# Kernel optimization log

Hardware: AMD Instinct MI355X
Metric: run time of the kernel (lower is better)

Reference implementation:

```python
import jax, jax.numpy as jnp
import numpy as np

N, E, DN, DE, H = 50000, 800000, 64, 64, 128


def setup_inputs() -> dict:
    key = jax.random.key(0)
    ks = jax.random.split(key, 12)
    s = 0.05
    return {
        "h": jax.random.normal(ks[0], (N, DN), jnp.float32),
        "eh": jax.random.normal(ks[1], (E, DE), jnp.float32),
        "W_node1": jax.random.normal(ks[2], (DN, H), jnp.float32) * s,
        "b_node1": jax.random.normal(ks[3], (H,), jnp.float32) * s,
        "W_node2": jax.random.normal(ks[4], (H, H), jnp.float32) * s,
        "W_edge1": jax.random.normal(ks[5], (DE, H), jnp.float32) * s,
        "b_edge1": jax.random.normal(ks[6], (H,), jnp.float32) * s,
        "W_edge2": jax.random.normal(ks[7], (H, H), jnp.float32) * s,
        "W_comb": jax.random.normal(ks[8], (H, DN), jnp.float32) * s,
        "W_ue": jax.random.normal(ks[9], (DN, DE), jnp.float32) * s,
        "src": jax.random.randint(ks[10], (E,), 0, N, jnp.int32),
        "dst": jax.random.randint(ks[11], (E,), 0, N, jnp.int32),
    }


def reference(h, eh, W_node1, b_node1, W_node2, W_edge1, b_edge1, W_edge2, W_comb, W_ue, src, dst):
    # gather per-edge endpoint node features: [E, DN]
    hs = h[src]
    hd = h[dst]
    # edge update: h_e = 0.8*h_e + 0.2 * fc_update_edge(h_src * h_dst)
    eh_new = 0.8 * eh + 0.2 * ((hs * hd) @ W_ue)
    # message: two small MLPs then tanh-combine, all per edge
    m1 = jax.nn.relu(hs @ W_node1 + b_node1) @ W_node2       # [E, H]
    m2 = jax.nn.relu(eh_new @ W_edge1 + b_edge1) @ W_edge2   # [E, H]
    m = jnp.tanh((m1 * m2) @ W_comb)                          # [E, DN]
    # reduce: scatter-sum messages to destination nodes + residual
    agg = jax.ops.segment_sum(m, dst, num_segments=h.shape[0])
    return agg + h
```

## Files before the change

kernel.cpp:

```cpp
#include <hip/hip_runtime.h>
#include <hip/hip_bf16.h>

#define NN 50000
#define NE 800000
#define DNODE 64
#define HD 128

typedef __attribute__((ext_vector_type(8)))  short bf16x8;
typedef __attribute__((ext_vector_type(16))) float f32x16;
typedef __attribute__((ext_vector_type(4)))  float f32x4;
typedef __attribute__((ext_vector_type(4)))  unsigned short u16x4;

__device__ __forceinline__ short f2bf(float f) {
    __hip_bfloat16 b = __float2bfloat16(f);
    unsigned short u;
    __builtin_memcpy(&u, &b, 2);
    return (short)u;
}
__device__ __forceinline__ float bf2f(unsigned short s) {
    return __uint_as_float(((unsigned)s) << 16);
}
__device__ __forceinline__ f32x16 zero16() {
    f32x16 z;
#pragma unroll
    for (int i = 0; i < 16; ++i) z[i] = 0.f;
    return z;
}

__device__ __forceinline__ unsigned cvt_pk(float lo, float hi) {
    unsigned r;
    asm("v_cvt_pk_bf16_f32 %0, %1, %2" : "=v"(r) : "v"(lo), "v"(hi));
    return r;
}

__device__ __forceinline__ bf16x8 pack_swap(const float* v) {
    unsigned w0 = cvt_pk(v[0], v[1]);
    unsigned w1 = cvt_pk(v[2], v[3]);
    unsigned w2 = cvt_pk(v[4], v[5]);
    unsigned w3 = cvt_pk(v[6], v[7]);
    asm("v_permlane32_swap_b32 %0, %1" : "+v"(w0), "+v"(w2));
    asm("v_permlane32_swap_b32 %0, %1" : "+v"(w1), "+v"(w3));
    union { unsigned u[4]; bf16x8 f; } o;
    o.u[0] = w0; o.u[1] = w1; o.u[2] = w2; o.u[3] = w3;
    return o.f;
}

__device__ __forceinline__ void build_frags(const float* __restrict__ W, int ncols,
                                            int nks, int nct, bf16x8* dst,
                                            int tid, int nthr) {
    int total = nct * nks * 64;
    for (int p = tid; p < total; p += nthr) {
        int fi = p >> 6, l = p & 63;
        int ct = fi / nks, ks = fi - ct * nks;
        int col = 32 * ct + (l & 31);
        int kb  = 16 * ks + 8 * (l >> 5);
        bf16x8 v;
#pragma unroll
        for (int j = 0; j < 8; ++j) v[j] = f2bf(W[(size_t)(kb + j) * ncols + col]);
        dst[p] = v;
    }
}

__global__ __launch_bounds__(512, 4) void node_kernel(
        const float* __restrict__ h, const float* __restrict__ Wn1,
        const float* __restrict__ bn1, const float* __restrict__ Wn2,
        unsigned short* __restrict__ M1, float* __restrict__ out, int ntiles) {
    __shared__ bf16x8 fWn1[16 * 64];
    __shared__ bf16x8 fWn2[32 * 64];
    __shared__ float  bias[HD];

    int tid = threadIdx.x;
    build_frags(Wn1, HD, 4, 4, fWn1, tid, 512);
    build_frags(Wn2, HD, 8, 4, fWn2, tid, 512);
    if (tid < HD) bias[tid] = bn1[tid];
    __syncthreads();

    int wv = tid >> 6, lane = tid & 63;
    int la = lane & 31, hh = lane >> 5;

    int tile = blockIdx.x * 8 + wv;
    if (tile >= ntiles) return;
    int n0 = tile * 32;
    int n_la = n0 + la;
    int nc = n_la < NN ? n_la : NN - 1;

    bf16x8 hfrag[4];
#pragma unroll
    for (int ks = 0; ks < 4; ++ks) {
        int cb = 16 * ks + 8 * hh;
        f32x4 h0 = *(const f32x4*)&h[(size_t)nc * DNODE + cb];
        f32x4 h1 = *(const f32x4*)&h[(size_t)nc * DNODE + cb + 4];
        if (n_la < NN) {
            *(f32x4*)&out[(size_t)n_la * DNODE + cb]     = h0;
            *(f32x4*)&out[(size_t)n_la * DNODE + cb + 4] = h1;
        }
        union { unsigned u[4]; bf16x8 f; } xf;
        xf.u[0] = cvt_pk(h0[0], h0[1]);
        xf.u[1] = cvt_pk(h0[2], h0[3]);
        xf.u[2] = cvt_pk(h1[0], h1[1]);
        xf.u[3] = cvt_pk(h1[2], h1[3]);
        hfrag[ks] = xf.f;
    }

    bf16x8 tfrag[8];
#pragma unroll
    for (int ct = 0; ct < 4; ++ct) {
        f32x16 acc = zero16();
#pragma unroll
        for (int ks = 0; ks < 4; ++ks)
            acc = __builtin_amdgcn_mfma_f32_32x32x16_bf16(fWn1[(ct * 4 + ks) * 64 + lane], hfrag[ks], acc, 0, 0, 0);
        float vals[16];
#pragma unroll
        for (int m = 0; m < 4; ++m) {
            f32x4 bv = *(const f32x4*)&bias[32 * ct + 8 * m + 4 * hh];
#pragma unroll
            for (int j = 0; j < 4; ++j)
                vals[4 * m + j] = fmaxf(acc[4 * m + j] + bv[j], 0.f);
        }
        tfrag[2 * ct]     = pack_swap(&vals[0]);
        tfrag[2 * ct + 1] = pack_swap(&vals[8]);
    }

#pragma unroll
    for (int ct = 0; ct < 4; ++ct) {
        f32x16 acc = zero16();
#pragma unroll
        for (int ks = 0; ks < 8; ++ks)
            acc = __builtin_amdgcn_mfma_f32_32x32x16_bf16(tfrag[ks], fWn2[(ct * 8 + ks) * 64 + lane], acc, 0, 0, 0);
#pragma unroll
        for (int r = 0; r < 16; ++r) {
            int row = (r & 3) + 8 * (r >> 2) + 4 * hh;
            int node = n0 + row;
            if (node < NN)
                M1[(size_t)node * HD + 32 * ct + la] = (unsigned short)f2bf(acc[r]);
        }
    }
}

__global__ __launch_bounds__(512, 4) void edge_kernel(
        const float* __restrict__ h, const float* __restrict__ eh,
        const float* __restrict__ Wue, const float* __restrict__ We1,
        const float* __restrict__ be1, const float* __restrict__ We2,
        const float* __restrict__ Wcb, const int* __restrict__ src,
        const int* __restrict__ dst, const unsigned short* __restrict__ M1,
        float* __restrict__ out) {
    __shared__ bf16x8 fUe[8 * 64];
    __shared__ bf16x8 fE1[16 * 64];
    __shared__ bf16x8 fE2[32 * 64];
    __shared__ bf16x8 fCb[16 * 64];
    __shared__ float  bias[HD];

    int tid = threadIdx.x;
    build_frags(Wue, 64, 4, 2, fUe, tid, 512);
    build_frags(We1, HD, 4, 4, fE1, tid, 512);
    build_frags(We2, HD, 8, 4, fE2, tid, 512);
    build_frags(Wcb, 64, 8, 2, fCb, tid, 512);
    if (tid < HD) bias[tid] = be1[tid];
    __syncthreads();

    int wv = tid >> 6, lane = tid & 63;
    int la = lane & 31, hh = lane >> 5;

    const int NT = NE / 32;
    int gw = blockIdx.x * 8 + wv;
    int t0 = (int)(((long long)gw * NT) >> 12);
    int t1 = (int)(((long long)(gw + 1) * NT) >> 12);

    for (int t = t0; t < t1; ++t) {
        int e0 = t * 32;
        int e_la = e0 + la;
        int srcA = src[e_la];
        int dstA = dst[e_la];

        f32x16 accU0 = zero16(), accU1 = zero16();
#pragma unroll
        for (int ks = 0; ks < 4; ++ks) {
            int cb = 16 * ks + 8 * hh;
            f32x4 s0 = *(const f32x4*)&h[(size_t)srcA * DNODE + cb];
            f32x4 s1 = *(const f32x4*)&h[(size_t)srcA * DNODE + cb + 4];
            f32x4 d0 = *(const f32x4*)&h[(size_t)dstA * DNODE + cb];
            f32x4 d1 = *(const f32x4*)&h[(size_t)dstA * DNODE + cb + 4];
            union { unsigned u[4]; bf16x8 f; } xf;
            xf.u[0] = cvt_pk(s0[0] * d0[0], s0[1] * d0[1]);
            xf.u[1] = cvt_pk(s0[2] * d0[2], s0[3] * d0[3]);
            xf.u[2] = cvt_pk(s1[0] * d1[0], s1[1] * d1[1]);
            xf.u[3] = cvt_pk(s1[2] * d1[2], s1[3] * d1[3]);
            accU0 = __builtin_amdgcn_mfma_f32_32x32x16_bf16(fUe[(0 * 4 + ks) * 64 + lane], xf.f, accU0, 0, 0, 0);
            accU1 = __builtin_amdgcn_mfma_f32_32x32x16_bf16(fUe[(1 * 4 + ks) * 64 + lane], xf.f, accU1, 0, 0, 0);
        }

        bf16x8 efrag[4];
#pragma unroll
        for (int ct = 0; ct < 2; ++ct) {
            const f32x16& aU = ct ? accU1 : accU0;
            float vals[16];
#pragma unroll
            for (int m = 0; m < 4; ++m) {
                f32x4 ev = *(const f32x4*)&eh[(size_t)e_la * 64 + 32 * ct + 8 * m + 4 * hh];
#pragma unroll
                for (int j = 0; j < 4; ++j)
                    vals[4 * m + j] = 0.8f * ev[j] + 0.2f * aU[4 * m + j];
            }
            efrag[2 * ct]     = pack_swap(&vals[0]);
            efrag[2 * ct + 1] = pack_swap(&vals[8]);
        }

        bf16x8 tfrag[8];
#pragma unroll
        for (int ct = 0; ct < 4; ++ct) {
            f32x16 acc = zero16();
#pragma unroll
            for (int ks = 0; ks < 4; ++ks)
                acc = __builtin_amdgcn_mfma_f32_32x32x16_bf16(fE1[(ct * 4 + ks) * 64 + lane], efrag[ks], acc, 0, 0, 0);
            float vals[16];
#pragma unroll
            for (int m = 0; m < 4; ++m) {
                f32x4 bv = *(const f32x4*)&bias[32 * ct + 8 * m + 4 * hh];
#pragma unroll
                for (int j = 0; j < 4; ++j)
                    vals[4 * m + j] = fmaxf(acc[4 * m + j] + bv[j], 0.f);
            }
            tfrag[2 * ct]     = pack_swap(&vals[0]);
            tfrag[2 * ct + 1] = pack_swap(&vals[8]);
        }

        bf16x8 pfrag[8];
#pragma unroll
        for (int ct = 0; ct < 4; ++ct) {
            u16x4 mq[4];
#pragma unroll
            for (int m = 0; m < 4; ++m)
                mq[m] = *(const u16x4*)&M1[(size_t)srcA * HD + 32 * ct + 8 * m + 4 * hh];
            f32x16 acc = zero16();
#pragma unroll
            for (int ks = 0; ks < 8; ++ks)
                acc = __builtin_amdgcn_mfma_f32_32x32x16_bf16(fE2[(ct * 8 + ks) * 64 + lane], tfrag[ks], acc, 0, 0, 0);
            float vals[16];
#pragma unroll
            for (int m = 0; m < 4; ++m)
#pragma unroll
                for (int j = 0; j < 4; ++j)
                    vals[4 * m + j] = acc[4 * m + j] * bf2f(mq[m][j]);
            pfrag[2 * ct]     = pack_swap(&vals[0]);
            pfrag[2 * ct + 1] = pack_swap(&vals[8]);
        }

        int dstR[16];
#pragma unroll
        for (int r = 0; r < 16; ++r)
            dstR[r] = __shfl(dstA, (r & 3) + 8 * (r >> 2) + 4 * hh);

#pragma unroll
        for (int ct = 0; ct < 2; ++ct) {
            f32x16 acc = zero16();
#pragma unroll
            for (int ks = 0; ks < 8; ++ks)
                acc = __builtin_amdgcn_mfma_f32_32x32x16_bf16(pfrag[ks], fCb[(ct * 8 + ks) * 64 + lane], acc, 0, 0, 0);
#pragma unroll
            for (int r = 0; r < 16; ++r) {
                float x = acc[r];
                x = fminf(fmaxf(x, -10.f), 10.f);
                float ex = __expf(2.f * x);
                float m = (ex - 1.f) * __builtin_amdgcn_rcpf(ex + 1.f);
                unsafeAtomicAdd(&out[(size_t)dstR[r] * DNODE + 32 * ct + la], m);
            }
        }
    }
}

extern "C" void kernel_launch(void* const* d_in, const int* in_sizes, int n_in,
                              void* d_out, int out_size, void* d_ws, size_t ws_size,
                              hipStream_t stream) {
    const float* h   = (const float*)d_in[0];
    const float* eh  = (const float*)d_in[1];
    const float* Wn1 = (const float*)d_in[2];
    const float* bn1 = (const float*)d_in[3];
    const float* Wn2 = (const float*)d_in[4];
    const float* We1 = (const float*)d_in[5];
    const float* be1 = (const float*)d_in[6];
    const float* We2 = (const float*)d_in[7];
    const float* Wcb = (const float*)d_in[8];
    const float* Wue = (const float*)d_in[9];
    const int*   src = (const int*)d_in[10];
    const int*   dst = (const int*)d_in[11];
    float* out = (float*)d_out;
    unsigned short* M1 = (unsigned short*)d_ws;

    int ntiles = (NN + 31) / 32;
    node_kernel<<<(ntiles + 7) / 8, 512, 0, stream>>>(h, Wn1, bn1, Wn2, M1, out, ntiles);
    edge_kernel<<<512, 512, 0, stream>>>(h, eh, Wue, We1, be1, We2, Wcb, src, dst, M1, out);
}
```

Before: 519.1 us.

## Scatter messages with packed bf16 atomics into scratch buffer, add residual after

Replaces the per-element fp32 atomic scatter with packed bf16 atomic adds into a zeroed bf16 accumulator. Lane pairs exchange values so each atomic covers two adjacent columns, which halves the atomic count. A new combine kernel adds the residual h and writes the output. The edge loop now prefetches the next tile's src/dst indices and issues the M1 and eh loads early. The cost is accumulating up to roughly 16 messages per node in bf16, which loses precision, plus an extra memset and kernel launch.

```diff
diff --git a/kernel.cpp b/kernel.cpp
--- a/kernel.cpp
+++ b/kernel.cpp
@@ -10,6 +10,7 @@
 typedef __attribute__((ext_vector_type(16))) float f32x16;
 typedef __attribute__((ext_vector_type(4)))  float f32x4;
 typedef __attribute__((ext_vector_type(4)))  unsigned short u16x4;
+typedef __attribute__((ext_vector_type(8)))  unsigned short u16x8;
 
 __device__ __forceinline__ short f2bf(float f) {
     __hip_bfloat16 b = __float2bfloat16(f);
@@ -31,6 +32,11 @@
     unsigned r;
     asm("v_cvt_pk_bf16_f32 %0, %1, %2" : "=v"(r) : "v"(lo), "v"(hi));
     return r;
+}
+
+__device__ __forceinline__ void atomic_pk_bf16(unsigned short* addr, unsigned data) {
+    unsigned long long a = (unsigned long long)(uintptr_t)addr;
+    asm volatile("global_atomic_pk_add_bf16 %0, %1, off" :: "v"(a), "v"(data) : "memory");
 }
 
 __device__ __forceinline__ bf16x8 pack_swap(const float* v) {
@@ -64,7 +70,7 @@
 __global__ __launch_bounds__(512, 4) void node_kernel(
         const float* __restrict__ h, const float* __restrict__ Wn1,
         const float* __restrict__ bn1, const float* __restrict__ Wn2,
-        unsigned short* __restrict__ M1, float* __restrict__ out, int ntiles) {
+        unsigned short* __restrict__ M1, int ntiles) {
     __shared__ bf16x8 fWn1[16 * 64];
     __shared__ bf16x8 fWn2[32 * 64];
     __shared__ float  bias[HD];
@@ -90,10 +96,6 @@
         int cb = 16 * ks + 8 * hh;
         f32x4 h0 = *(const f32x4*)&h[(size_t)nc * DNODE + cb];
         f32x4 h1 = *(const f32x4*)&h[(size_t)nc * DNODE + cb + 4];
-        if (n_la < NN) {
-            *(f32x4*)&out[(size_t)n_la * DNODE + cb]     = h0;
-            *(f32x4*)&out[(size_t)n_la * DNODE + cb + 4] = h1;
-        }
         union { unsigned u[4]; bf16x8 f; } xf;
         xf.u[0] = cvt_pk(h0[0], h0[1]);
         xf.u[1] = cvt_pk(h0[2], h0[3]);
@@ -143,7 +145,7 @@
         const float* __restrict__ be1, const float* __restrict__ We2,
         const float* __restrict__ Wcb, const int* __restrict__ src,
         const int* __restrict__ dst, const unsigned short* __restrict__ M1,
-        float* __restrict__ out) {
+        unsigned short* __restrict__ Macc) {
     __shared__ bf16x8 fUe[8 * 64];
     __shared__ bf16x8 fE1[16 * 64];
     __shared__ bf16x8 fE2[32 * 64];
@@ -165,12 +167,29 @@
     int gw = blockIdx.x * 8 + wv;
     int t0 = (int)(((long long)gw * NT) >> 12);
     int t1 = (int)(((long long)(gw + 1) * NT) >> 12);
+    if (t0 >= t1) return;
+
+    int srcA = src[t0 * 32 + la];
+    int dstA = dst[t0 * 32 + la];
 
     for (int t = t0; t < t1; ++t) {
-        int e0 = t * 32;
-        int e_la = e0 + la;
-        int srcA = src[e_la];
-        int dstA = dst[e_la];
+        int e_la = t * 32 + la;
+        int eN = (t + 1 < t1) ? (t + 1) * 32 + la : e_la;
+        int srcN = src[eN];
+        int dstN = dst[eN];
+
+        u16x4 mq[16];
+#pragma unroll
+        for (int ct = 0; ct < 4; ++ct)
+#pragma unroll
+            for (int m = 0; m < 4; ++m)
+                mq[4 * ct + m] = *(const u16x4*)&M1[(size_t)srcA * HD + 32 * ct + 8 * m + 4 * hh];
+        f32x4 ehq[8];
+#pragma unroll
+        for (int ct = 0; ct < 2; ++ct)
+#pragma unroll
+            for (int m = 0; m < 4; ++m)
+                ehq[4 * ct + m] = *(const f32x4*)&eh[(size_t)e_la * 64 + 32 * ct + 8 * m + 4 * hh];
 
         f32x16 accU0 = zero16(), accU1 = zero16();
 #pragma unroll
@@ -195,12 +214,10 @@
             const f32x16& aU = ct ? accU1 : accU0;
             float vals[16];
 #pragma unroll
-            for (int m = 0; m < 4; ++m) {
-                f32x4 ev = *(const f32x4*)&eh[(size_t)e_la * 64 + 32 * ct + 8 * m + 4 * hh];
+            for (int m = 0; m < 4; ++m)
 #pragma unroll
                 for (int j = 0; j < 4; ++j)
-                    vals[4 * m + j] = 0.8f * ev[j] + 0.2f * aU[4 * m + j];
-            }
+                    vals[4 * m + j] = 0.8f * ehq[4 * ct + m][j] + 0.2f * aU[4 * m + j];
             efrag[2 * ct]     = pack_swap(&vals[0]);
             efrag[2 * ct + 1] = pack_swap(&vals[8]);
         }
@@ -227,10 +244,6 @@
         bf16x8 pfrag[8];
 #pragma unroll
         for (int ct = 0; ct < 4; ++ct) {
-            u16x4 mq[4];
-#pragma unroll
-            for (int m = 0; m < 4; ++m)
-                mq[m] = *(const u16x4*)&M1[(size_t)srcA * HD + 32 * ct + 8 * m + 4 * hh];
             f32x16 acc = zero16();
 #pragma unroll
             for (int ks = 0; ks < 8; ++ks)
@@ -240,7 +253,7 @@
             for (int m = 0; m < 4; ++m)
 #pragma unroll
                 for (int j = 0; j < 4; ++j)
-                    vals[4 * m + j] = acc[4 * m + j] * bf2f(mq[m][j]);
+                    vals[4 * m + j] = acc[4 * m + j] * bf2f(mq[4 * ct + m][j]);
             pfrag[2 * ct]     = pack_swap(&vals[0]);
             pfrag[2 * ct + 1] = pack_swap(&vals[8]);
         }
@@ -250,22 +263,48 @@
         for (int r = 0; r < 16; ++r)
             dstR[r] = __shfl(dstA, (r & 3) + 8 * (r >> 2) + 4 * hh);
 
-#pragma unroll
-        for (int ct = 0; ct < 2; ++ct) {
-            f32x16 acc = zero16();
-#pragma unroll
-            for (int ks = 0; ks < 8; ++ks)
-                acc = __builtin_amdgcn_mfma_f32_32x32x16_bf16(pfrag[ks], fCb[(ct * 8 + ks) * 64 + lane], acc, 0, 0, 0);
-#pragma unroll
-            for (int r = 0; r < 16; ++r) {
-                float x = acc[r];
-                x = fminf(fmaxf(x, -10.f), 10.f);
-                float ex = __expf(2.f * x);
-                float m = (ex - 1.f) * __builtin_amdgcn_rcpf(ex + 1.f);
-                unsafeAtomicAdd(&out[(size_t)dstR[r] * DNODE + 32 * ct + la], m);
-            }
-        }
-    }
+        f32x16 accF0 = zero16(), accF1 = zero16();
+#pragma unroll
+        for (int ks = 0; ks < 8; ++ks) {
+            accF0 = __builtin_amdgcn_mfma_f32_32x32x16_bf16(pfrag[ks], fCb[(0 * 8 + ks) * 64 + lane], accF0, 0, 0, 0);
+            accF1 = __builtin_amdgcn_mfma_f32_32x32x16_bf16(pfrag[ks], fCb[(1 * 8 + ks) * 64 + lane], accF1, 0, 0, 0);
+        }
+        int odd = lane & 1;
+#pragma unroll
+        for (int r = 0; r < 16; ++r) {
+            float x0 = fminf(fmaxf(accF0[r], -10.f), 10.f);
+            float x1 = fminf(fmaxf(accF1[r], -10.f), 10.f);
+            float ex0 = __expf(2.f * x0), ex1 = __expf(2.f * x1);
+            float m0 = (ex0 - 1.f) * __builtin_amdgcn_rcpf(ex0 + 1.f);
+            float m1 = (ex1 - 1.f) * __builtin_amdgcn_rcpf(ex1 + 1.f);
+            float e0 = __shfl_xor(m0, 1);
+            float e1 = __shfl_xor(m1, 1);
+            unsigned w = odd ? cvt_pk(e1, m1) : cvt_pk(m0, e0);
+            int colstart = odd ? (31 + la) : la;
+            atomic_pk_bf16(&Macc[(size_t)dstR[r] * 64 + colstart], w);
+        }
+
+        srcA = srcN;
+        dstA = dstN;
+    }
+}
+
+__global__ __launch_bounds__(256) void combine_kernel(
+        const float* __restrict__ h, const unsigned short* __restrict__ Macc,
+        float* __restrict__ out) {
+    int i = (blockIdx.x * 256 + threadIdx.x) * 8;
+    if (i >= NN * DNODE) return;
+    u16x8 mv = *(const u16x8*)&Macc[i];
+    f32x4 h0 = *(const f32x4*)&h[i];
+    f32x4 h1 = *(const f32x4*)&h[i + 4];
+    f32x4 o0, o1;
+#pragma unroll
+    for (int j = 0; j < 4; ++j) {
+        o0[j] = h0[j] + bf2f(mv[j]);
+        o1[j] = h1[j] + bf2f(mv[4 + j]);
+    }
+    *(f32x4*)&out[i]     = o0;
+    *(f32x4*)&out[i + 4] = o1;
 }
 
 extern "C" void kernel_launch(void* const* d_in, const int* in_sizes, int n_in,
@@ -284,9 +323,13 @@
     const int*   src = (const int*)d_in[10];
     const int*   dst = (const int*)d_in[11];
     float* out = (float*)d_out;
-    unsigned short* M1 = (unsigned short*)d_ws;
-
+
+    unsigned short* M1   = (unsigned short*)d_ws;
+    unsigned short* Macc = (unsigned short*)((char*)d_ws + (size_t)NN * HD * 2);
+
+    hipMemsetAsync(Macc, 0, (size_t)NN * DNODE * 2, stream);
     int ntiles = (NN + 31) / 32;
-    node_kernel<<<(ntiles + 7) / 8, 512, 0, stream>>>(h, Wn1, bn1, Wn2, M1, out, ntiles);
-    edge_kernel<<<512, 512, 0, stream>>>(h, eh, Wue, We1, be1, We2, Wcb, src, dst, M1, out);
-}
+    node_kernel<<<(ntiles + 7) / 8, 512, 0, stream>>>(h, Wn1, bn1, Wn2, M1, ntiles);
+    edge_kernel<<<512, 512, 0, stream>>>(h, eh, Wue, We1, be1, We2, Wcb, src, dst, M1, Macc);
+    combine_kernel<<<(NN * DNODE / 8 + 255) / 256, 256, 0, stream>>>(h, Macc, out);
+}
```

Result: faster. 478.0 us (-7.9%).
